# Kernel optimization log

Measured on AMD Instinct MI355X. Metric: run time of the kernel, lower is better.

The kernel has to match this reference:

```python
import jax, jax.numpy as jnp
import numpy as np
from jax import lax

# Mamba hyperparams (mamba_ssm defaults for d_model=768)
D_MODEL = 768
N_LAYER = 8
D_INNER = 2 * D_MODEL          # 1536
D_STATE = 16
DT_RANK = D_MODEL // 16        # 48
D_CONV = 4
BATCH = 4
SEQLEN = 1024


def _ln(x, w, b):
    mu = jnp.mean(x, axis=-1, keepdims=True)
    var = jnp.mean(jnp.square(x - mu), axis=-1, keepdims=True)
    return (x - mu) * lax.rsqrt(var + 1e-5) * w + b


def _silu(x):
    return x * jax.nn.sigmoid(x)


def _mamba_mixer(h, in_proj, conv_w, conv_b, x_proj, dt_w, dt_b, A_log, Dv, out_proj):
    # h: [B, L, d_model]
    xz = jnp.einsum('bld,ed->ble', h, in_proj)          # [B, L, 2*d_inner]
    xm, z = jnp.split(xz, 2, axis=-1)
    # causal depthwise conv1d over time
    xc = lax.conv_general_dilated(
        xm.transpose(0, 2, 1), conv_w, (1,), [(D_CONV - 1, 0)],
        feature_group_count=D_INNER)                    # [B, d_inner, L]
    u = _silu((xc + conv_b[None, :, None]).transpose(0, 2, 1))  # [B, L, d_inner]
    dbc = jnp.einsum('bld,ed->ble', u, x_proj)          # [B, L, dt_rank+2*d_state]
    dt = jax.nn.softplus(jnp.einsum('blr,dr->bld', dbc[..., :DT_RANK], dt_w) + dt_b)
    Bm = dbc[..., DT_RANK:DT_RANK + D_STATE]            # [B, L, d_state]
    Cm = dbc[..., DT_RANK + D_STATE:]                   # [B, L, d_state]
    A = -jnp.exp(A_log)                                 # [d_inner, d_state]

    def step(hstate, inp):
        dt_t, B_t, u_t, C_t = inp                       # [B,d_inner],[B,d_state],[B,d_inner],[B,d_state]
        dA = jnp.exp(dt_t[..., None] * A)               # [B, d_inner, d_state]
        hstate = dA * hstate + (dt_t * u_t)[..., None] * B_t[:, None, :]
        y = jnp.einsum('bds,bs->bd', hstate, C_t)
        return hstate, y

    h0 = jnp.zeros((h.shape[0], D_INNER, D_STATE), h.dtype)
    _, ys = lax.scan(step, h0, (dt.transpose(1, 0, 2), Bm.transpose(1, 0, 2),
                                u.transpose(1, 0, 2), Cm.transpose(1, 0, 2)))
    y = ys.transpose(1, 0, 2) + u * Dv                  # skip connection D*u
    y = y * _silu(z)
    return jnp.einsum('ble,de->bld', y, out_proj)


def setup_inputs() -> dict:
    key = jax.random.key(0)
    ks = jax.random.split(key, 16)
    f32 = jnp.float32
    d = {
        'x': jax.random.normal(ks[0], (BATCH, SEQLEN, D_MODEL), f32),
        'pos': jax.random.normal(ks[1], (BATCH, SEQLEN, D_MODEL), f32),
        'norm_w': jnp.ones((N_LAYER, D_MODEL), f32),
        'norm_b': jnp.zeros((N_LAYER, D_MODEL), f32),
        'in_proj': jax.random.normal(ks[2], (N_LAYER, 2 * D_INNER, D_MODEL), f32) * 0.02,
        'conv_w': jax.random.normal(ks[3], (N_LAYER, D_INNER, 1, D_CONV), f32) * 0.2,
        'conv_b': jnp.zeros((N_LAYER, D_INNER), f32),
        'x_proj': jax.random.normal(ks[4], (N_LAYER, DT_RANK + 2 * D_STATE, D_INNER), f32) * 0.02,
        'dt_w': jax.random.normal(ks[5], (N_LAYER, D_INNER, DT_RANK), f32) * 0.1,
        'dt_b': jax.random.uniform(ks[6], (N_LAYER, D_INNER), f32, -4.0, -2.0),
        'A_log': jnp.broadcast_to(jnp.log(jnp.arange(1, D_STATE + 1, dtype=f32)),
                                  (N_LAYER, D_INNER, D_STATE)).copy(),
        'Dv': jnp.ones((N_LAYER, D_INNER), f32),
        'out_proj': jax.random.normal(ks[7], (N_LAYER, D_MODEL, D_INNER), f32) * 0.02,
        'normf_w': jnp.ones((D_MODEL,), f32),
        'normf_b': jnp.zeros((D_MODEL,), f32),
        'dec_w': jnp.ones((D_MODEL,), f32),
        'dec_b': jnp.zeros((D_MODEL,), f32),
        'return_token_num': 256,
    }
    return d


def reference(x, pos, norm_w, norm_b, in_proj, conv_w, conv_b, x_proj, dt_w, dt_b,
              A_log, Dv, out_proj, normf_w, normf_b, dec_w, dec_b, return_token_num):
    hidden = x + pos
    residual = None
    for l in range(N_LAYER):
        residual = hidden if residual is None else hidden + residual
        h = _ln(residual, norm_w[l], norm_b[l])
        hidden = _mamba_mixer(h, in_proj[l], conv_w[l], conv_b[l], x_proj[l],
                              dt_w[l], dt_b[l], A_log[l], Dv[l], out_proj[l])
    residual = hidden + residual
    hidden = _ln(residual, normf_w, normf_b)
    return _ln(hidden[:, -return_token_num:], dec_w, dec_b)
```

## Files before the change

kernel.cpp:

```cpp
#include <hip/hip_runtime.h>
#include <math.h>

#define D_MODEL 768
#define N_LAYER 8
#define D_INNER 1536
#define D_STATE 16
#define DT_RANK 48
#define D_CONV  4
#define BATCH   4
#define SEQLEN  1024
#define NTOK    (BATCH*SEQLEN)
#define DBC_W   (DT_RANK + 2*D_STATE)
#define NC      64
#define CHUNK_T (SEQLEN/NC)
#define XP_KS   16
#define XP_KSL  (D_INNER/XP_KS)
#define CONV_TCH 16
#define OP_KS   4

typedef __attribute__((ext_vector_type(8))) short short8v;
typedef __attribute__((ext_vector_type(4))) float float4v;

__device__ __forceinline__ void split_bf16(float x, short& hi, short& lo) {
  unsigned u = __float_as_uint(x);
  unsigned r = (u + 0x7fffu + ((u >> 16) & 1u)) >> 16;
  hi = (short)r;
  float fhi = __uint_as_float(r << 16);
  float xl = x - fhi;
  unsigned u2 = __float_as_uint(xl);
  unsigned r2 = (u2 + 0x7fffu + ((u2 >> 16) & 1u)) >> 16;
  lo = (short)r2;
}

__device__ __forceinline__ void gload16(const short* g, short* l) {
  __builtin_amdgcn_global_load_lds(
      (const __attribute__((address_space(1))) void*)g,
      (__attribute__((address_space(3))) void*)l, 16, 0, 0);
}

__global__ __launch_bounds__(256) void split_kernel(
    const float* __restrict__ src, short* __restrict__ hi,
    short* __restrict__ lo, int n4) {
  int stride = gridDim.x * 256;
  for (int i = blockIdx.x * 256 + threadIdx.x; i < n4; i += stride) {
    float4 v = ((const float4*)src)[i];
    short4 h, g;
    split_bf16(v.x, h.x, g.x);
    split_bf16(v.y, h.y, g.y);
    split_bf16(v.z, h.z, g.z);
    split_bf16(v.w, h.w, g.w);
    ((short4*)hi)[i] = h;
    ((short4*)lo)[i] = g;
  }
}

__global__ __launch_bounds__(256) void ln_kernel(
    const float* __restrict__ x, const float* __restrict__ pos,
    float* __restrict__ resid, const float* __restrict__ opart,
    short* __restrict__ hh_hi, short* __restrict__ hh_lo,
    const float* __restrict__ w, const float* __restrict__ b, int first) {
  int row = blockIdx.x;
  int tid = threadIdx.x;
  int base = row * D_MODEL;
  __shared__ float red[256];
  __shared__ float s_mu, s_rs;
  float v[3];
#pragma unroll
  for (int i = 0; i < 3; ++i) {
    int c = tid + i * 256;
    float r;
    if (first) {
      r = x[base + c] + pos[base + c];
    } else {
      float hysum = opart[base + c];
#pragma unroll
      for (int k = 1; k < OP_KS; ++k)
        hysum += opart[(size_t)k * NTOK * D_MODEL + base + c];
      r = resid[base + c] + hysum;
    }
    resid[base + c] = r;
    v[i] = r;
  }
  float s = v[0] + v[1] + v[2];
  red[tid] = s; __syncthreads();
  for (int off = 128; off > 0; off >>= 1) {
    if (tid < off) red[tid] += red[tid + off];
    __syncthreads();
  }
  if (tid == 0) s_mu = red[0] / D_MODEL;
  __syncthreads();
  float mu = s_mu;
  float q = 0.f;
#pragma unroll
  for (int i = 0; i < 3; ++i) { float d = v[i] - mu; q += d * d; }
  __syncthreads();
  red[tid] = q; __syncthreads();
  for (int off = 128; off > 0; off >>= 1) {
    if (tid < off) red[tid] += red[tid + off];
    __syncthreads();
  }
  if (tid == 0) s_rs = rsqrtf(red[0] / D_MODEL + 1e-5f);
  __syncthreads();
  float rs = s_rs;
#pragma unroll
  for (int i = 0; i < 3; ++i) {
    int c = tid + i * 256;
    float val = (v[i] - mu) * rs * w[c] + b[c];
    short hv, lv; split_bf16(val, hv, lv);
    hh_hi[base + c] = hv;
    hh_lo[base + c] = lv;
  }
}

__global__ __launch_bounds__(256) void gemm_bf16x3(
    const short* __restrict__ Ahi, const short* __restrict__ Alo, int lda,
    const short* __restrict__ Bhi, const short* __restrict__ Blo, int ldb,
    float* __restrict__ C, int M, int N, int K) {
  const int BK = 32;
  __shared__ short Ash[128][32];
  __shared__ short Asl[128][32];
  __shared__ short Bsh[128][32];
  __shared__ short Bsl[128][32];
  int brow = blockIdx.y * 128;
  int bcol = blockIdx.x * 128;
  int ksl = K / gridDim.z;
  int kbeg = blockIdx.z * ksl;
  int kend = kbeg + ksl;
  float* Cw = C + (size_t)blockIdx.z * M * N;
  int tid = threadIdx.x;
  int wv = tid >> 6, l = tid & 63;
  int wr = (wv >> 1) * 64;
  int wc = (wv & 1) * 64;
  int lrow = l & 15;
  int rslot = ((l >> 4) ^ ((l >> 1) & 3)) * 8;
  int lr = l >> 2;
  int lp = l & 3;
  float4v zero = {0.f, 0.f, 0.f, 0.f};
  float4v acc[4][4];
#pragma unroll
  for (int m = 0; m < 4; ++m)
#pragma unroll
    for (int n = 0; n < 4; ++n) acc[m][n] = zero;

  for (int k0 = kbeg; k0 < kend; k0 += BK) {
#pragma unroll
    for (int half = 0; half < 2; ++half) {
      int row = wv * 32 + half * 16 + lr;
      int s = lp ^ ((row >> 1) & 3);
      int ldsrow = wv * 32 + half * 16;
      size_t ao = (size_t)(brow + row) * lda + k0 + s * 8;
      size_t bo = (size_t)(bcol + row) * ldb + k0 + s * 8;
      gload16(Ahi + ao, &Ash[ldsrow][0]);
      gload16(Alo + ao, &Asl[ldsrow][0]);
      gload16(Bhi + bo, &Bsh[ldsrow][0]);
      gload16(Blo + bo, &Bsl[ldsrow][0]);
    }
    __syncthreads();
    short8v ah[4], al[4];
#pragma unroll
    for (int m = 0; m < 4; ++m) {
      int R = wr + m * 16 + lrow;
      ah[m] = *(const short8v*)&Ash[R][rslot];
      al[m] = *(const short8v*)&Asl[R][rslot];
    }
#pragma unroll
    for (int n = 0; n < 4; ++n) {
      int R = wc + n * 16 + lrow;
      short8v bh = *(const short8v*)&Bsh[R][rslot];
      short8v bl = *(const short8v*)&Bsl[R][rslot];
#pragma unroll
      for (int m = 0; m < 4; ++m) {
        acc[m][n] = __builtin_amdgcn_mfma_f32_16x16x32_bf16(ah[m], bh, acc[m][n], 0, 0, 0);
        acc[m][n] = __builtin_amdgcn_mfma_f32_16x16x32_bf16(ah[m], bl, acc[m][n], 0, 0, 0);
        acc[m][n] = __builtin_amdgcn_mfma_f32_16x16x32_bf16(al[m], bh, acc[m][n], 0, 0, 0);
      }
    }
    __syncthreads();
  }
  int drow = (l >> 4) * 4, dcol = l & 15;
#pragma unroll
  for (int m = 0; m < 4; ++m)
#pragma unroll
    for (int n = 0; n < 4; ++n)
#pragma unroll
      for (int j = 0; j < 4; ++j)
        Cw[(size_t)(brow + wr + m * 16 + drow + j) * N + bcol + wc + n * 16 + dcol] =
            acc[m][n][j];
}

__global__ __launch_bounds__(256) void xproj_gemm(
    const float* __restrict__ u, const float* __restrict__ xp,
    float* __restrict__ part) {
  const int BM = 64, BK = 32;
  __shared__ __align__(16) float As[BK][BM + 4];
  __shared__ float Bs[BK][DBC_W + 1];
  int brow = blockIdx.x * BM;
  int kbase = blockIdx.y * XP_KSL;
  int tid = threadIdx.x;
  int tr = (tid / 16) * 4;
  int tc = (tid % 16) * 5;
  float acc[4][5] = {};
  for (int k0 = kbase; k0 < kbase + XP_KSL; k0 += BK) {
#pragma unroll
    for (int it = 0; it < 2; ++it) {
      int lin = tid + it * 256;
      int r  = lin >> 3;
      int kq = (lin & 7) * 4;
      float4 a = *(const float4*)&u[(size_t)(brow + r) * D_INNER + k0 + kq];
      As[kq + 0][r] = a.x; As[kq + 1][r] = a.y;
      As[kq + 2][r] = a.z; As[kq + 3][r] = a.w;
    }
#pragma unroll
    for (int it = 0; it < 3; ++it) {
      int lin = tid + it * 256;
      if (lin < 640) {
        int e  = lin >> 3;
        int kq = (lin & 7) * 4;
        float4 bv = *(const float4*)&xp[(size_t)e * D_INNER + k0 + kq];
        Bs[kq + 0][e] = bv.x; Bs[kq + 1][e] = bv.y;
        Bs[kq + 2][e] = bv.z; Bs[kq + 3][e] = bv.w;
      }
    }
    __syncthreads();
#pragma unroll
    for (int kk = 0; kk < BK; ++kk) {
      float4 av = *(const float4*)&As[kk][tr];
      float ar[4] = {av.x, av.y, av.z, av.w};
      float br[5];
#pragma unroll
      for (int j = 0; j < 5; ++j) br[j] = Bs[kk][tc + j];
#pragma unroll
      for (int i = 0; i < 4; ++i)
#pragma unroll
        for (int j = 0; j < 5; ++j) acc[i][j] += ar[i] * br[j];
    }
    __syncthreads();
  }
  float* dst = part + (size_t)blockIdx.y * NTOK * DBC_W;
#pragma unroll
  for (int i = 0; i < 4; ++i)
#pragma unroll
    for (int j = 0; j < 5; ++j)
      dst[(size_t)(brow + tr + i) * DBC_W + tc + j] = acc[i][j];
}

__global__ __launch_bounds__(256) void reduce_dbc_kernel(
    const float* __restrict__ part, float* __restrict__ dbc, int n4) {
  int i = blockIdx.x * 256 + threadIdx.x;
  if (i >= n4) return;
  float4 s = ((const float4*)part)[i];
#pragma unroll
  for (int k = 1; k < XP_KS; ++k) {
    float4 v = ((const float4*)(part + (size_t)k * NTOK * DBC_W))[i];
    s.x += v.x; s.y += v.y; s.z += v.z; s.w += v.w;
  }
  ((float4*)dbc)[i] = s;
}

__global__ __launch_bounds__(256) void conv_silu_kernel(
    const float* __restrict__ xz, const float* __restrict__ cw,
    const float* __restrict__ cb, float* __restrict__ u) {
  int idx = blockIdx.x * 256 + threadIdx.x;
  const int NTC = SEQLEN / CONV_TCH;
  if (idx >= BATCH * NTC * D_INNER) return;
  int c  = idx % D_INNER;
  int tc = (idx / D_INNER) % NTC;
  int b  = idx / (D_INNER * NTC);
  int t0 = tc * CONV_TCH;
  float w0 = cw[c * 4 + 0], w1 = cw[c * 4 + 1];
  float w2 = cw[c * 4 + 2], w3 = cw[c * 4 + 3];
  float bias = cb[c];
  const float* base = xz + (size_t)b * SEQLEN * (2 * D_INNER) + c;
  float xm3 = 0.f, xm2 = 0.f, xm1 = 0.f;
  if (t0 > 0) {
    xm3 = base[(size_t)(t0 - 3) * (2 * D_INNER)];
    xm2 = base[(size_t)(t0 - 2) * (2 * D_INNER)];
    xm1 = base[(size_t)(t0 - 1) * (2 * D_INNER)];
  }
  float* ub = u + (size_t)(b * SEQLEN + t0) * D_INNER + c;
#pragma unroll
  for (int i = 0; i < CONV_TCH; ++i) {
    float xt = base[(size_t)(t0 + i) * (2 * D_INNER)];
    float acc = bias + xm3 * w0 + xm2 * w1 + xm1 * w2 + xt * w3;
    float sig = 1.f / (1.f + __expf(-acc));
    ub[(size_t)i * D_INNER] = acc * sig;
    xm3 = xm2; xm2 = xm1; xm1 = xt;
  }
}

__device__ __forceinline__ float softplusf(float a) {
  return (a > 20.f) ? a : log1pf(__expf(a));
}

__global__ __launch_bounds__(256) void scan_chunk1(
    float* __restrict__ dty, const float* __restrict__ u,
    const float* __restrict__ dbc, const float* __restrict__ A_log,
    const float* __restrict__ dtw, const float* __restrict__ dtb,
    float* __restrict__ S, float* __restrict__ dtsum) {
  int blk = blockIdx.x;
  int bcq = (blk * 256) / D_INNER;
  int d = blk * 256 - bcq * D_INNER + threadIdx.x;
  int c = bcq & (NC - 1);
  int b = bcq / NC;
  float A[D_STATE];
#pragma unroll
  for (int s = 0; s < D_STATE; ++s) A[s] = -__expf(A_log[d * D_STATE + s]);
  float w[DT_RANK];
  {
    const float4* w4 = (const float4*)(dtw + (size_t)d * DT_RANK);
#pragma unroll
    for (int j = 0; j < DT_RANK / 4; ++j) {
      float4 v = w4[j];
      w[j * 4 + 0] = v.x; w[j * 4 + 1] = v.y;
      w[j * 4 + 2] = v.z; w[j * 4 + 3] = v.w;
    }
  }
  float bias = dtb[d];
  float h[D_STATE];
#pragma unroll
  for (int s = 0; s < D_STATE; ++s) h[s] = 0.f;
  float dts = 0.f;
  int t0 = c * CHUNK_T;
  for (int t = t0; t < t0 + CHUNK_T; ++t) {
    size_t rowb = (size_t)b * SEQLEN + t;
    const float* bc = dbc + rowb * DBC_W;
    float raw = bias;
#pragma unroll
    for (int k = 0; k < DT_RANK; ++k) raw += bc[k] * w[k];
    float dtv = softplusf(raw);
    dty[rowb * D_INNER + d] = dtv;
    float uv  = u[rowb * D_INNER + d];
    float dtu = dtv * uv;
    dts += dtv;
#pragma unroll
    for (int s = 0; s < D_STATE; ++s) {
      float da = __expf(dtv * A[s]);
      h[s] = da * h[s] + dtu * bc[DT_RANK + s];
    }
  }
  size_t base = (((size_t)b * NC + c) * D_STATE) * D_INNER + d;
#pragma unroll
  for (int s = 0; s < D_STATE; ++s) S[base + (size_t)s * D_INNER] = h[s];
  dtsum[((size_t)b * NC + c) * D_INNER + d] = dts;
}

__global__ __launch_bounds__(256) void scan_combine(
    float* __restrict__ S, const float* __restrict__ dtsum,
    const float* __restrict__ A_log) {
  int g = blockIdx.x * 256 + threadIdx.x;
  if (g >= BATCH * D_STATE * D_INNER) return;
  int d = g % D_INNER;
  int s = (g / D_INNER) % D_STATE;
  int b = g / (D_INNER * D_STATE);
  float A = -__expf(A_log[d * D_STATE + s]);
  float h = 0.f;
  for (int c = 0; c < NC; ++c) {
    size_t off = (((size_t)b * NC + c) * D_STATE + s) * D_INNER + d;
    float dts = dtsum[((size_t)b * NC + c) * D_INNER + d];
    float Sv = S[off];
    S[off] = h;
    h = __expf(dts * A) * h + Sv;
  }
}

__global__ __launch_bounds__(256) void scan_chunk2(
    const float* __restrict__ dty, const float* __restrict__ u,
    const float* __restrict__ dbc, const float* __restrict__ xz,
    const float* __restrict__ A_log,
    const float* __restrict__ Dv, const float* __restrict__ hin,
    short* __restrict__ y_hi, short* __restrict__ y_lo) {
  int blk = blockIdx.x;
  int bcq = (blk * 256) / D_INNER;
  int d = blk * 256 - bcq * D_INNER + threadIdx.x;
  int c = bcq & (NC - 1);
  int b = bcq / NC;
  float A[D_STATE];
#pragma unroll
  for (int s = 0; s < D_STATE; ++s) A[s] = -__expf(A_log[d * D_STATE + s]);
  float Dval = Dv[d];
  float h[D_STATE];
  size_t hbase = (((size_t)b * NC + c) * D_STATE) * D_INNER + d;
#pragma unroll
  for (int s = 0; s < D_STATE; ++s) h[s] = hin[hbase + (size_t)s * D_INNER];
  int t0 = c * CHUNK_T;
  for (int t = t0; t < t0 + CHUNK_T; ++t) {
    size_t rowb = (size_t)b * SEQLEN + t;
    const float* bc = dbc + rowb * DBC_W;
    float dtv = dty[rowb * D_INNER + d];
    float uv  = u[rowb * D_INNER + d];
    float dtu = dtv * uv;
    float yv = 0.f;
#pragma unroll
    for (int s = 0; s < D_STATE; ++s) {
      float da = __expf(dtv * A[s]);
      h[s] = da * h[s] + dtu * bc[DT_RANK + s];
      yv += h[s] * bc[DT_RANK + D_STATE + s];
    }
    float zv = xz[rowb * (2 * D_INNER) + D_INNER + d];
    float sig = 1.f / (1.f + __expf(-zv));
    float yo = (yv + uv * Dval) * (zv * sig);
    short hv, lv; split_bf16(yo, hv, lv);
    y_hi[rowb * D_INNER + d] = hv;
    y_lo[rowb * D_INNER + d] = lv;
  }
}

__global__ __launch_bounds__(256) void final_kernel(
    const float* __restrict__ opart, const float* __restrict__ resid,
    const float* __restrict__ fw, const float* __restrict__ fb,
    const float* __restrict__ dw, const float* __restrict__ db,
    float* __restrict__ out, int rtn) {
  int rowo = blockIdx.x;
  int b = rowo / rtn;
  int t = SEQLEN - rtn + (rowo % rtn);
  int tid = threadIdx.x;
  size_t base = ((size_t)b * SEQLEN + t) * D_MODEL;
  __shared__ float red[256];
  __shared__ float s_mu1, s_rs1, s_mu2, s_rs2;
  float v[3];
#pragma unroll
  for (int i = 0; i < 3; ++i) {
    int c = tid + i * 256;
    float hysum = opart[base + c];
#pragma unroll
    for (int k = 1; k < OP_KS; ++k)
      hysum += opart[(size_t)k * NTOK * D_MODEL + base + c];
    v[i] = hysum + resid[base + c];
  }
  red[tid] = v[0] + v[1] + v[2]; __syncthreads();
  for (int off = 128; off > 0; off >>= 1) {
    if (tid < off) red[tid] += red[tid + off];
    __syncthreads();
  }
  if (tid == 0) s_mu1 = red[0] / D_MODEL;
  __syncthreads();
  float mu = s_mu1, q = 0.f;
#pragma unroll
  for (int i = 0; i < 3; ++i) { float dd = v[i] - mu; q += dd * dd; }
  __syncthreads();
  red[tid] = q; __syncthreads();
  for (int off = 128; off > 0; off >>= 1) {
    if (tid < off) red[tid] += red[tid + off];
    __syncthreads();
  }
  if (tid == 0) s_rs1 = rsqrtf(red[0] / D_MODEL + 1e-5f);
  __syncthreads();
  float rs = s_rs1;
#pragma unroll
  for (int i = 0; i < 3; ++i) {
    int c = tid + i * 256;
    v[i] = (v[i] - mu) * rs * fw[c] + fb[c];
  }
  __syncthreads();
  red[tid] = v[0] + v[1] + v[2]; __syncthreads();
  for (int off = 128; off > 0; off >>= 1) {
    if (tid < off) red[tid] += red[tid + off];
    __syncthreads();
  }
  if (tid == 0) s_mu2 = red[0] / D_MODEL;
  __syncthreads();
  mu = s_mu2; q = 0.f;
#pragma unroll
  for (int i = 0; i < 3; ++i) { float dd = v[i] - mu; q += dd * dd; }
  __syncthreads();
  red[tid] = q; __syncthreads();
  for (int off = 128; off > 0; off >>= 1) {
    if (tid < off) red[tid] += red[tid + off];
    __syncthreads();
  }
  if (tid == 0) s_rs2 = rsqrtf(red[0] / D_MODEL + 1e-5f);
  __syncthreads();
  rs = s_rs2;
#pragma unroll
  for (int i = 0; i < 3; ++i) {
    int c = tid + i * 256;
    out[(size_t)rowo * D_MODEL + c] = (v[i] - mu) * rs * dw[c] + db[c];
  }
}

extern "C" void kernel_launch(void* const* d_in, const int* in_sizes, int n_in,
                              void* d_out, int out_size, void* d_ws, size_t ws_size,
                              hipStream_t stream) {
  const float* x       = (const float*)d_in[0];
  const float* pos     = (const float*)d_in[1];
  const float* norm_w  = (const float*)d_in[2];
  const float* norm_b  = (const float*)d_in[3];
  const float* in_proj = (const float*)d_in[4];
  const float* conv_w  = (const float*)d_in[5];
  const float* conv_b  = (const float*)d_in[6];
  const float* x_proj  = (const float*)d_in[7];
  const float* dt_w    = (const float*)d_in[8];
  const float* dt_b    = (const float*)d_in[9];
  const float* A_log   = (const float*)d_in[10];
  const float* Dv      = (const float*)d_in[11];
  const float* out_proj= (const float*)d_in[12];
  const float* normf_w = (const float*)d_in[13];
  const float* normf_b = (const float*)d_in[14];
  const float* dec_w   = (const float*)d_in[15];
  const float* dec_b   = (const float*)d_in[16];
  int rtn = out_size / (BATCH * D_MODEL);

  const size_t WI = (size_t)2 * D_INNER * D_MODEL;
  const size_t WO = (size_t)D_MODEL * D_INNER;

  float* ws    = (float*)d_ws;
  float* resid = ws;
  float* xz    = resid + (size_t)NTOK * D_MODEL;
  float* u     = xz    + (size_t)NTOK * 2 * D_INNER;
  float* dbc   = u     + (size_t)NTOK * D_INNER;
  float* dty   = dbc   + (size_t)NTOK * DBC_W;
  float* Sbuf  = dty   + (size_t)NTOK * D_INNER;
  float* dtsum = Sbuf  + (size_t)BATCH * NC * D_STATE * D_INNER;
  float* dbcp  = Sbuf;
  short* hh_hi = (short*)(dtsum + (size_t)BATCH * NC * D_INNER);
  short* hh_lo = hh_hi + (size_t)NTOK * D_MODEL;
  short* y_hi  = hh_lo + (size_t)NTOK * D_MODEL;
  short* y_lo  = y_hi  + (size_t)NTOK * D_INNER;
  short* wIh   = y_lo  + (size_t)NTOK * D_INNER;
  short* wIl   = wIh + N_LAYER * WI;
  short* wOh   = wIl + N_LAYER * WI;
  short* wOl   = wOh + N_LAYER * WO;
  float* opart = xz;

  split_kernel<<<2048, 256, 0, stream>>>(in_proj, wIh, wIl,
                                         (int)(N_LAYER * WI / 4));
  split_kernel<<<2048, 256, 0, stream>>>(out_proj, wOh, wOl,
                                         (int)(N_LAYER * WO / 4));

  for (int l = 0; l < N_LAYER; ++l) {
    ln_kernel<<<NTOK, 256, 0, stream>>>(x, pos, resid, opart, hh_hi, hh_lo,
        norm_w + l * D_MODEL, norm_b + l * D_MODEL, l == 0);

    dim3 g1(2 * D_INNER / 128, NTOK / 128, 1);
    gemm_bf16x3<<<g1, 256, 0, stream>>>(hh_hi, hh_lo, D_MODEL,
        wIh + l * WI, wIl + l * WI, D_MODEL, xz, NTOK, 2 * D_INNER, D_MODEL);

    int convtot = BATCH * (SEQLEN / CONV_TCH) * D_INNER;
    conv_silu_kernel<<<(convtot + 255) / 256, 256, 0, stream>>>(
        xz, conv_w + (size_t)l * D_INNER * D_CONV, conv_b + l * D_INNER, u);

    dim3 gxp(NTOK / 64, XP_KS);
    xproj_gemm<<<gxp, 256, 0, stream>>>(
        u, x_proj + (size_t)l * DBC_W * D_INNER, dbcp);
    reduce_dbc_kernel<<<(NTOK * DBC_W / 4 + 255) / 256, 256, 0, stream>>>(
        dbcp, dbc, NTOK * DBC_W / 4);

    const float* Al = A_log + (size_t)l * D_INNER * D_STATE;
    int tot1 = BATCH * NC * D_INNER;
    scan_chunk1<<<tot1 / 256, 256, 0, stream>>>(
        dty, u, dbc, Al, dt_w + (size_t)l * D_INNER * DT_RANK,
        dt_b + (size_t)l * D_INNER, Sbuf, dtsum);
    scan_combine<<<(BATCH * D_STATE * D_INNER + 255) / 256, 256, 0, stream>>>(
        Sbuf, dtsum, Al);
    scan_chunk2<<<tot1 / 256, 256, 0, stream>>>(
        dty, u, dbc, xz, Al, Dv + l * D_INNER, Sbuf, y_hi, y_lo);

    dim3 g2(D_MODEL / 128, NTOK / 128, OP_KS);
    gemm_bf16x3<<<g2, 256, 0, stream>>>(y_hi, y_lo, D_INNER,
        wOh + l * WO, wOl + l * WO, D_INNER, opart, NTOK, D_MODEL, D_INNER);
  }

  final_kernel<<<BATCH * rtn, 256, 0, stream>>>(
      opart, resid, normf_w, normf_b, dec_w, dec_b, (float*)d_out, rtn);
}
```

Measured before the change: 2.139 ms.

## Vectorize LN and conv kernels; recompute dt in scan pass two

The layernorm, final and conv+SiLU kernels now use float4 loads and stores: one float4 per thread for a 768-wide row, and four channels per thread in the conv. The scan no longer writes a dt buffer in its first pass and reads it back in the second. Instead the second pass recomputes the dt projection and softplus from dbc and dt_w. This trades a 4096x1536 float write plus read per layer for 48 extra FMAs per timestep in scan_chunk2, along with extra register pressure from the 48-element weight array.

```diff
diff --git a/kernel.cpp b/kernel.cpp
--- a/kernel.cpp
+++ b/kernel.cpp
@@ -61,28 +61,31 @@
     const float* __restrict__ w, const float* __restrict__ b, int first) {
   int row = blockIdx.x;
   int tid = threadIdx.x;
-  int base = row * D_MODEL;
+  size_t base4 = (size_t)row * (D_MODEL / 4);
   __shared__ float red[256];
   __shared__ float s_mu, s_rs;
-  float v[3];
-#pragma unroll
-  for (int i = 0; i < 3; ++i) {
-    int c = tid + i * 256;
-    float r;
+  float4 v = make_float4(0.f, 0.f, 0.f, 0.f);
+  bool act = tid < D_MODEL / 4;
+  if (act) {
     if (first) {
-      r = x[base + c] + pos[base + c];
+      float4 a = ((const float4*)x)[base4 + tid];
+      float4 p = ((const float4*)pos)[base4 + tid];
+      v = make_float4(a.x + p.x, a.y + p.y, a.z + p.z, a.w + p.w);
     } else {
-      float hysum = opart[base + c];
-#pragma unroll
-      for (int k = 1; k < OP_KS; ++k)
-        hysum += opart[(size_t)k * NTOK * D_MODEL + base + c];
-      r = resid[base + c] + hysum;
-    }
-    resid[base + c] = r;
-    v[i] = r;
-  }
-  float s = v[0] + v[1] + v[2];
-  red[tid] = s; __syncthreads();
+      float4 r = ((const float4*)resid)[base4 + tid];
+      float4 o = ((const float4*)opart)[base4 + tid];
+      float4 s = make_float4(o.x, o.y, o.z, o.w);
+#pragma unroll
+      for (int k = 1; k < OP_KS; ++k) {
+        float4 o2 = ((const float4*)opart)[(size_t)k * (NTOK * D_MODEL / 4) + base4 + tid];
+        s.x += o2.x; s.y += o2.y; s.z += o2.z; s.w += o2.w;
+      }
+      v = make_float4(r.x + s.x, r.y + s.y, r.z + s.z, r.w + s.w);
+    }
+    ((float4*)resid)[base4 + tid] = v;
+  }
+  red[tid] = act ? (v.x + v.y + v.z + v.w) : 0.f;
+  __syncthreads();
   for (int off = 128; off > 0; off >>= 1) {
     if (tid < off) red[tid] += red[tid + off];
     __syncthreads();
@@ -91,8 +94,10 @@
   __syncthreads();
   float mu = s_mu;
   float q = 0.f;
-#pragma unroll
-  for (int i = 0; i < 3; ++i) { float d = v[i] - mu; q += d * d; }
+  if (act) {
+    float dx = v.x - mu, dy = v.y - mu, dz = v.z - mu, dw = v.w - mu;
+    q = dx * dx + dy * dy + dz * dz + dw * dw;
+  }
   __syncthreads();
   red[tid] = q; __syncthreads();
   for (int off = 128; off > 0; off >>= 1) {
@@ -102,13 +107,18 @@
   if (tid == 0) s_rs = rsqrtf(red[0] / D_MODEL + 1e-5f);
   __syncthreads();
   float rs = s_rs;
-#pragma unroll
-  for (int i = 0; i < 3; ++i) {
-    int c = tid + i * 256;
-    float val = (v[i] - mu) * rs * w[c] + b[c];
-    short hv, lv; split_bf16(val, hv, lv);
-    hh_hi[base + c] = hv;
-    hh_lo[base + c] = lv;
+  if (act) {
+    float4 wv = ((const float4*)w)[tid];
+    float4 bv = ((const float4*)b)[tid];
+    float o0 = (v.x - mu) * rs * wv.x + bv.x;
+    float o1 = (v.y - mu) * rs * wv.y + bv.y;
+    float o2 = (v.z - mu) * rs * wv.z + bv.z;
+    float o3 = (v.w - mu) * rs * wv.w + bv.w;
+    short4 h, g;
+    split_bf16(o0, h.x, g.x); split_bf16(o1, h.y, g.y);
+    split_bf16(o2, h.z, g.z); split_bf16(o3, h.w, g.w);
+    ((short4*)hh_hi)[base4 + tid] = h;
+    ((short4*)hh_lo)[base4 + tid] = g;
   }
 }
 
@@ -262,28 +272,43 @@
     const float* __restrict__ cb, float* __restrict__ u) {
   int idx = blockIdx.x * 256 + threadIdx.x;
   const int NTC = SEQLEN / CONV_TCH;
-  if (idx >= BATCH * NTC * D_INNER) return;
-  int c  = idx % D_INNER;
-  int tc = (idx / D_INNER) % NTC;
-  int b  = idx / (D_INNER * NTC);
+  const int C4 = D_INNER / 4;
+  if (idx >= BATCH * NTC * C4) return;
+  int c4 = idx % C4;
+  int tc = (idx / C4) % NTC;
+  int b  = idx / (C4 * NTC);
   int t0 = tc * CONV_TCH;
-  float w0 = cw[c * 4 + 0], w1 = cw[c * 4 + 1];
-  float w2 = cw[c * 4 + 2], w3 = cw[c * 4 + 3];
-  float bias = cb[c];
-  const float* base = xz + (size_t)b * SEQLEN * (2 * D_INNER) + c;
-  float xm3 = 0.f, xm2 = 0.f, xm1 = 0.f;
+  int c = c4 * 4;
+  float4 w0 = ((const float4*)cw)[c + 0];
+  float4 w1 = ((const float4*)cw)[c + 1];
+  float4 w2 = ((const float4*)cw)[c + 2];
+  float4 w3 = ((const float4*)cw)[c + 3];
+  float4 bias = ((const float4*)cb)[c4];
+  const float4* base = (const float4*)(xz + (size_t)b * SEQLEN * (2 * D_INNER)) + c4;
+  const int STR = 2 * D_INNER / 4;
+  float4 xm3 = make_float4(0.f, 0.f, 0.f, 0.f);
+  float4 xm2 = xm3, xm1 = xm3;
   if (t0 > 0) {
-    xm3 = base[(size_t)(t0 - 3) * (2 * D_INNER)];
-    xm2 = base[(size_t)(t0 - 2) * (2 * D_INNER)];
-    xm1 = base[(size_t)(t0 - 1) * (2 * D_INNER)];
-  }
-  float* ub = u + (size_t)(b * SEQLEN + t0) * D_INNER + c;
+    xm3 = base[(size_t)(t0 - 3) * STR];
+    xm2 = base[(size_t)(t0 - 2) * STR];
+    xm1 = base[(size_t)(t0 - 1) * STR];
+  }
+  float4* ub = (float4*)(u + (size_t)(b * SEQLEN + t0) * D_INNER) + c4;
+  const int USTR = D_INNER / 4;
 #pragma unroll
   for (int i = 0; i < CONV_TCH; ++i) {
-    float xt = base[(size_t)(t0 + i) * (2 * D_INNER)];
-    float acc = bias + xm3 * w0 + xm2 * w1 + xm1 * w2 + xt * w3;
-    float sig = 1.f / (1.f + __expf(-acc));
-    ub[(size_t)i * D_INNER] = acc * sig;
+    float4 xt = base[(size_t)(t0 + i) * STR];
+    float4 a;
+    a.x = bias.x + xm3.x * w0.x + xm2.x * w0.y + xm1.x * w0.z + xt.x * w0.w;
+    a.y = bias.y + xm3.y * w1.x + xm2.y * w1.y + xm1.y * w1.z + xt.y * w1.w;
+    a.z = bias.z + xm3.z * w2.x + xm2.z * w2.y + xm1.z * w2.z + xt.z * w2.w;
+    a.w = bias.w + xm3.w * w3.x + xm2.w * w3.y + xm1.w * w3.z + xt.w * w3.w;
+    float4 o;
+    o.x = a.x / (1.f + __expf(-a.x));
+    o.y = a.y / (1.f + __expf(-a.y));
+    o.z = a.z / (1.f + __expf(-a.z));
+    o.w = a.w / (1.f + __expf(-a.w));
+    ub[(size_t)i * USTR] = o;
     xm3 = xm2; xm2 = xm1; xm1 = xt;
   }
 }
@@ -293,7 +318,7 @@
 }
 
 __global__ __launch_bounds__(256) void scan_chunk1(
-    float* __restrict__ dty, const float* __restrict__ u,
+    const float* __restrict__ u,
     const float* __restrict__ dbc, const float* __restrict__ A_log,
     const float* __restrict__ dtw, const float* __restrict__ dtb,
     float* __restrict__ S, float* __restrict__ dtsum) {
@@ -328,7 +353,6 @@
 #pragma unroll
     for (int k = 0; k < DT_RANK; ++k) raw += bc[k] * w[k];
     float dtv = softplusf(raw);
-    dty[rowb * D_INNER + d] = dtv;
     float uv  = u[rowb * D_INNER + d];
     float dtu = dtv * uv;
     dts += dtv;
@@ -364,9 +388,10 @@
 }
 
 __global__ __launch_bounds__(256) void scan_chunk2(
-    const float* __restrict__ dty, const float* __restrict__ u,
+    const float* __restrict__ u,
     const float* __restrict__ dbc, const float* __restrict__ xz,
     const float* __restrict__ A_log,
+    const float* __restrict__ dtw, const float* __restrict__ dtb,
     const float* __restrict__ Dv, const float* __restrict__ hin,
     short* __restrict__ y_hi, short* __restrict__ y_lo) {
   int blk = blockIdx.x;
@@ -377,6 +402,17 @@
   float A[D_STATE];
 #pragma unroll
   for (int s = 0; s < D_STATE; ++s) A[s] = -__expf(A_log[d * D_STATE + s]);
+  float w[DT_RANK];
+  {
+    const float4* w4 = (const float4*)(dtw + (size_t)d * DT_RANK);
+#pragma unroll
+    for (int j = 0; j < DT_RANK / 4; ++j) {
+      float4 v = w4[j];
+      w[j * 4 + 0] = v.x; w[j * 4 + 1] = v.y;
+      w[j * 4 + 2] = v.z; w[j * 4 + 3] = v.w;
+    }
+  }
+  float bias = dtb[d];
   float Dval = Dv[d];
   float h[D_STATE];
   size_t hbase = (((size_t)b * NC + c) * D_STATE) * D_INNER + d;
@@ -386,7 +422,10 @@
   for (int t = t0; t < t0 + CHUNK_T; ++t) {
     size_t rowb = (size_t)b * SEQLEN + t;
     const float* bc = dbc + rowb * DBC_W;
-    float dtv = dty[rowb * D_INNER + d];
+    float raw = bias;
+#pragma unroll
+    for (int k = 0; k < DT_RANK; ++k) raw += bc[k] * w[k];
+    float dtv = softplusf(raw);
     float uv  = u[rowb * D_INNER + d];
     float dtu = dtv * uv;
     float yv = 0.f;
@@ -414,20 +453,24 @@
   int b = rowo / rtn;
   int t = SEQLEN - rtn + (rowo % rtn);
   int tid = threadIdx.x;
-  size_t base = ((size_t)b * SEQLEN + t) * D_MODEL;
+  size_t base4 = ((size_t)b * SEQLEN + t) * (D_MODEL / 4);
   __shared__ float red[256];
   __shared__ float s_mu1, s_rs1, s_mu2, s_rs2;
-  float v[3];
-#pragma unroll
-  for (int i = 0; i < 3; ++i) {
-    int c = tid + i * 256;
-    float hysum = opart[base + c];
-#pragma unroll
-    for (int k = 1; k < OP_KS; ++k)
-      hysum += opart[(size_t)k * NTOK * D_MODEL + base + c];
-    v[i] = hysum + resid[base + c];
-  }
-  red[tid] = v[0] + v[1] + v[2]; __syncthreads();
+  bool act = tid < D_MODEL / 4;
+  float4 v = make_float4(0.f, 0.f, 0.f, 0.f);
+  if (act) {
+    float4 o = ((const float4*)opart)[base4 + tid];
+    float4 s = make_float4(o.x, o.y, o.z, o.w);
+#pragma unroll
+    for (int k = 1; k < OP_KS; ++k) {
+      float4 o2 = ((const float4*)opart)[(size_t)k * (NTOK * D_MODEL / 4) + base4 + tid];
+      s.x += o2.x; s.y += o2.y; s.z += o2.z; s.w += o2.w;
+    }
+    float4 r = ((const float4*)resid)[base4 + tid];
+    v = make_float4(r.x + s.x, r.y + s.y, r.z + s.z, r.w + s.w);
+  }
+  red[tid] = act ? (v.x + v.y + v.z + v.w) : 0.f;
+  __syncthreads();
   for (int off = 128; off > 0; off >>= 1) {
     if (tid < off) red[tid] += red[tid + off];
     __syncthreads();
@@ -435,8 +478,10 @@
   if (tid == 0) s_mu1 = red[0] / D_MODEL;
   __syncthreads();
   float mu = s_mu1, q = 0.f;
-#pragma unroll
-  for (int i = 0; i < 3; ++i) { float dd = v[i] - mu; q += dd * dd; }
+  if (act) {
+    float dx = v.x - mu, dy = v.y - mu, dz = v.z - mu, dww = v.w - mu;
+    q = dx * dx + dy * dy + dz * dz + dww * dww;
+  }
   __syncthreads();
   red[tid] = q; __syncthreads();
   for (int off = 128; off > 0; off >>= 1) {
@@ -446,13 +491,17 @@
   if (tid == 0) s_rs1 = rsqrtf(red[0] / D_MODEL + 1e-5f);
   __syncthreads();
   float rs = s_rs1;
-#pragma unroll
-  for (int i = 0; i < 3; ++i) {
-    int c = tid + i * 256;
-    v[i] = (v[i] - mu) * rs * fw[c] + fb[c];
-  }
-  __syncthreads();
-  red[tid] = v[0] + v[1] + v[2]; __syncthreads();
+  if (act) {
+    float4 wv = ((const float4*)fw)[tid];
+    float4 bv = ((const float4*)fb)[tid];
+    v.x = (v.x - mu) * rs * wv.x + bv.x;
+    v.y = (v.y - mu) * rs * wv.y + bv.y;
+    v.z = (v.z - mu) * rs * wv.z + bv.z;
+    v.w = (v.w - mu) * rs * wv.w + bv.w;
+  }
+  __syncthreads();
+  red[tid] = act ? (v.x + v.y + v.z + v.w) : 0.f;
+  __syncthreads();
   for (int off = 128; off > 0; off >>= 1) {
     if (tid < off) red[tid] += red[tid + off];
     __syncthreads();
@@ -460,8 +509,10 @@
   if (tid == 0) s_mu2 = red[0] / D_MODEL;
   __syncthreads();
   mu = s_mu2; q = 0.f;
-#pragma unroll
-  for (int i = 0; i < 3; ++i) { float dd = v[i] - mu; q += dd * dd; }
+  if (act) {
+    float dx = v.x - mu, dy = v.y - mu, dz = v.z - mu, dww = v.w - mu;
+    q = dx * dx + dy * dy + dz * dz + dww * dww;
+  }
   __syncthreads();
   red[tid] = q; __syncthreads();
   for (int off = 128; off > 0; off >>= 1) {
@@ -471,10 +522,15 @@
   if (tid == 0) s_rs2 = rsqrtf(red[0] / D_MODEL + 1e-5f);
   __syncthreads();
   rs = s_rs2;
-#pragma unroll
-  for (int i = 0; i < 3; ++i) {
-    int c = tid + i * 256;
-    out[(size_t)rowo * D_MODEL + c] = (v[i] - mu) * rs * dw[c] + db[c];
+  if (act) {
+    float4 wv = ((const float4*)dw)[tid];
+    float4 bv = ((const float4*)db)[tid];
+    float4 o;
+    o.x = (v.x - mu) * rs * wv.x + bv.x;
+    o.y = (v.y - mu) * rs * wv.y + bv.y;
+    o.z = (v.z - mu) * rs * wv.z + bv.z;
+    o.w = (v.w - mu) * rs * wv.w + bv.w;
+    ((float4*)out)[(size_t)rowo * (D_MODEL / 4) + tid] = o;
   }
 }
 
@@ -508,8 +564,7 @@
   float* xz    = resid + (size_t)NTOK * D_MODEL;
   float* u     = xz    + (size_t)NTOK * 2 * D_INNER;
   float* dbc   = u     + (size_t)NTOK * D_INNER;
-  float* dty   = dbc   + (size_t)NTOK * DBC_W;
-  float* Sbuf  = dty   + (size_t)NTOK * D_INNER;
+  float* Sbuf  = dbc   + (size_t)NTOK * DBC_W;
   float* dtsum = Sbuf  + (size_t)BATCH * NC * D_STATE * D_INNER;
   float* dbcp  = Sbuf;
   short* hh_hi = (short*)(dtsum + (size_t)BATCH * NC * D_INNER);
@@ -535,7 +590,7 @@
     gemm_bf16x3<<<g1, 256, 0, stream>>>(hh_hi, hh_lo, D_MODEL,
         wIh + l * WI, wIl + l * WI, D_MODEL, xz, NTOK, 2 * D_INNER, D_MODEL);
 
-    int convtot = BATCH * (SEQLEN / CONV_TCH) * D_INNER;
+    int convtot = BATCH * (SEQLEN / CONV_TCH) * (D_INNER / 4);
     conv_silu_kernel<<<(convtot + 255) / 256, 256, 0, stream>>>(
         xz, conv_w + (size_t)l * D_INNER * D_CONV, conv_b + l * D_INNER, u);
 
@@ -546,14 +601,15 @@
         dbcp, dbc, NTOK * DBC_W / 4);
 
     const float* Al = A_log + (size_t)l * D_INNER * D_STATE;
+    const float* dtwl = dt_w + (size_t)l * D_INNER * DT_RANK;
+    const float* dtbl = dt_b + (size_t)l * D_INNER;
     int tot1 = BATCH * NC * D_INNER;
     scan_chunk1<<<tot1 / 256, 256, 0, stream>>>(
-        dty, u, dbc, Al, dt_w + (size_t)l * D_INNER * DT_RANK,
-        dt_b + (size_t)l * D_INNER, Sbuf, dtsum);
+        u, dbc, Al, dtwl, dtbl, Sbuf, dtsum);
     scan_combine<<<(BATCH * D_STATE * D_INNER + 255) / 256, 256, 0, stream>>>(
         Sbuf, dtsum, Al);
     scan_chunk2<<<tot1 / 256, 256, 0, stream>>>(
-        dty, u, dbc, xz, Al, Dv + l * D_INNER, Sbuf, y_hi, y_lo);
+        u, dbc, xz, Al, dtwl, dtbl, Dv + l * D_INNER, Sbuf, y_hi, y_lo);
 
     dim3 g2(D_MODEL / 128, NTOK / 128, OP_KS);
     gemm_bf16x3<<<g2, 256, 0, stream>>>(y_hi, y_lo, D_INNER,
```

After: 2.410 ms. 1.13x slower.
